# Kernel tuning notes

Measured on AMD Instinct MI355X. Metric: run time of the kernel, lower is better.

The kernel has to match this reference:

```python
import jax, jax.numpy as jnp
import numpy as np

EPS = 1e-5

def _bn(x, gamma, beta, axes):
    # batch-norm with batch statistics (torch training-mode forward, biased var)
    mu = jnp.mean(x, axis=axes, keepdims=True)
    var = jnp.var(x, axis=axes, keepdims=True)
    shape = [1] * x.ndim
    shape[1] = -1  # channel dim is axis 1
    return (x - mu) * jax.lax.rsqrt(var + EPS) * gamma.reshape(shape) + beta.reshape(shape)

def setup_inputs() -> dict:
    key = jax.random.key(0)
    k1, k2, k3, k4, k5 = jax.random.split(key, 5)
    N, H, D, L, M, C = 8, 8, 64, 1024, 1024, 64
    scale = 1.0 / np.sqrt(D)
    return {
        "query": jax.random.normal(k1, (N, H, D, L), dtype=jnp.float32) * scale,
        "key": jax.random.normal(k2, (N, H, D, M), dtype=jnp.float32) * scale,
        "value": jax.random.normal(k3, (N, H, C, M), dtype=jnp.float32),
        "gamma_sim": jnp.ones((H,), dtype=jnp.float32),
        "beta_sim": jnp.zeros((H,), dtype=jnp.float32),
        "gamma_v": jnp.ones((H * C,), dtype=jnp.float32),
        "beta_v": jnp.zeros((H * C,), dtype=jnp.float32),
    }

def reference(query, key, value, gamma_sim, beta_sim, gamma_v, beta_v):
    N, H, D, L = query.shape
    C = value.shape[2]
    # QK^T -> [N, H, L, M]
    logits = jnp.einsum('bhdl,bhdm->bhlm', query, key)
    # BatchNorm2d over channel=head: stats over (N, L, M)
    logits = _bn(logits, gamma_sim, beta_sim, axes=(0, 2, 3))
    # softmax in fp32 (autocast(enabled=False) + .float())
    weights = jax.nn.softmax(logits.astype(jnp.float32), axis=-1)
    # AV -> [N, H, D_v, L] then flatten heads
    rv = jnp.einsum('bhlm,bhdm->bhdl', weights, value).reshape(N, H * C, L)
    # BatchNorm1d over channel: stats over (N, L)
    rv = _bn(rv, gamma_v, beta_v, axes=(0, 2))
    # torch F.gelu default is exact (erf-based)
    return jax.nn.gelu(rv, approximate=False)
```

## Files before the change

### kernel.cpp

```cpp
#include <hip/hip_runtime.h>
#include <hip/hip_bf16.h>
#include <math.h>


typedef __attribute__((ext_vector_type(4)))  float    f32x4;
typedef __attribute__((ext_vector_type(16))) float    f32x16;
typedef __attribute__((ext_vector_type(8)))  __bf16   bf16x8;
typedef __attribute__((ext_vector_type(8)))  short    s16x8;
typedef __attribute__((ext_vector_type(4)))  short    s16x4;
typedef __attribute__((ext_vector_type(2)))  unsigned u32x2;
typedef __attribute__((ext_vector_type(4)))  unsigned u32x4;

#define KT_OFF 0u
#define VB_OFF (8u*1024u*1024u)
#define P1_OFF (16u*1024u*1024u)
#define RS_OFF (24u*1024u*1024u)
#define SPLIT_WS_NEED (24u*1024u*1024u + 512u*1024u + 4096u)

static __device__ __forceinline__ short bf16s(float f) {
  return __builtin_bit_cast(short, (__bf16)f);
}
static __device__ __forceinline__ unsigned pkbf(float lo, float hi) {
  unsigned l = (unsigned)__builtin_bit_cast(unsigned short, (__bf16)lo);
  unsigned h = (unsigned)__builtin_bit_cast(unsigned short, (__bf16)hi);
  return l | (h << 16);
}
static __device__ __forceinline__ float bf2f(short s) {
  return __builtin_bit_cast(float, ((unsigned)(unsigned short)s) << 16);
}
static __device__ __forceinline__ bf16x8 cvt8(const float* p) {
  f32x4 a = *(const f32x4*)p;
  f32x4 b = *(const f32x4*)(p + 4);
  bf16x8 r;
  r[0]=(__bf16)a[0]; r[1]=(__bf16)a[1]; r[2]=(__bf16)a[2]; r[3]=(__bf16)a[3];
  r[4]=(__bf16)b[0]; r[5]=(__bf16)b[1]; r[6]=(__bf16)b[2]; r[7]=(__bf16)b[3];
  return r;
}
static __device__ __forceinline__ f32x16 z16() {
  f32x16 z;
  #pragma unroll
  for (int i = 0; i < 16; ++i) z[i] = 0.f;
  return z;
}
static __device__ __forceinline__ bf16x8 mk8(unsigned a, unsigned b, unsigned c, unsigned d) {
  u32x4 u; u[0]=a; u[1]=b; u[2]=c; u[3]=d;
  return __builtin_bit_cast(bf16x8, u);
}
static __device__ __forceinline__ void gll16(const void* g, void* l) {
  __builtin_amdgcn_global_load_lds(
      (const __attribute__((address_space(1))) void*)g,
      (__attribute__((address_space(3))) void*)l, 16, 0, 0);
}

__global__ __launch_bounds__(256) void k0_prep(const float* __restrict__ K,
                                               const float* __restrict__ V,
                                               short* __restrict__ Kt,
                                               short* __restrict__ Vb) {
  int tid = threadIdx.x;
  if (blockIdx.x < 1024) {
    int bh = blockIdx.x >> 4;
    int m0 = (blockIdx.x & 15) << 6;
    __shared__ short tile[64][72];
    int d = tid >> 2;
    #pragma unroll
    for (int it = 0; it < 4; ++it) {
      int mc4 = (tid & 3) + (it << 2);
      const f32x4 v = *(const f32x4*)(K + (((size_t)(bh*64 + d)) << 10) + m0 + (mc4 << 2));
      #pragma unroll
      for (int j = 0; j < 4; ++j) tile[mc4*4 + j][d] = bf16s(v[j]);
    }
    __syncthreads();
    int m = tid >> 2, q = tid & 3;
    s16x8 o0, o1;
    #pragma unroll
    for (int j = 0; j < 8; ++j) { o0[j] = tile[m][q*16 + j]; o1[j] = tile[m][q*16 + 8 + j]; }
    short* dst = Kt + ((size_t)bh << 16) + ((size_t)(m0 + m) << 6) + (q << 4);
    *(s16x8*)dst = o0;
    *(s16x8*)(dst + 8) = o1;
  } else {
    size_t base = ((size_t)(blockIdx.x - 1024)) << 13;
    #pragma unroll
    for (int it = 0; it < 8; ++it) {
      size_t idx = base + ((size_t)it << 10) + (tid << 2);
      f32x4 x = *(const f32x4*)(V + idx);
      s16x4 y;
      #pragma unroll
      for (int j = 0; j < 4; ++j) y[j] = bf16s(x[j]);
      *(s16x4*)(Vb + idx) = y;
    }
  }
}

__global__ __launch_bounds__(512) void k1_gram(const float* __restrict__ Q,
                                               const float* __restrict__ K,
                                               float* __restrict__ ss) {
  int bh = blockIdx.x;
  int tid = threadIdx.x, w = tid >> 6, lane = tid & 63;
  int l31 = lane & 31, hi = lane >> 5;
  const float* qlo = Q + ((size_t)bh << 16) + ((size_t)l31 << 10);
  const float* qhi = qlo + (32u << 10);
  const float* klo = K + ((size_t)bh << 16) + ((size_t)l31 << 10);
  const float* khi = klo + (32u << 10);
  f32x16 gq00 = z16(), gq01 = z16(), gq11 = z16();
  f32x16 gk00 = z16(), gk01 = z16(), gk11 = z16();
  for (int lc = 0; lc < 8; ++lc) {
    int loff = (w << 7) + (lc << 4) + (hi << 3);
    bf16x8 aql = cvt8(qlo + loff), aqh = cvt8(qhi + loff);
    bf16x8 akl = cvt8(klo + loff), akh = cvt8(khi + loff);
    gq00 = __builtin_amdgcn_mfma_f32_32x32x16_bf16(aql, aql, gq00, 0, 0, 0);
    gq01 = __builtin_amdgcn_mfma_f32_32x32x16_bf16(aql, aqh, gq01, 0, 0, 0);
    gq11 = __builtin_amdgcn_mfma_f32_32x32x16_bf16(aqh, aqh, gq11, 0, 0, 0);
    gk00 = __builtin_amdgcn_mfma_f32_32x32x16_bf16(akl, akl, gk00, 0, 0, 0);
    gk01 = __builtin_amdgcn_mfma_f32_32x32x16_bf16(akl, akh, gk01, 0, 0, 0);
    gk11 = __builtin_amdgcn_mfma_f32_32x32x16_bf16(akh, akh, gk11, 0, 0, 0);
  }
  __shared__ float RQ[8][64][16];
  __shared__ float RK[8][64][16];
  float part = 0.f;
  #define K1_REDUCE(GQ_, GK_, WT_)                                          \
    __syncthreads();                                                        \
    _Pragma("unroll")                                                       \
    for (int r = 0; r < 16; ++r) { RQ[w][lane][r] = GQ_[r]; RK[w][lane][r] = GK_[r]; } \
    __syncthreads();                                                        \
    if (tid < 256) {                                                        \
      int e = tid & 63, rq = (tid >> 6) << 2;                               \
      _Pragma("unroll")                                                     \
      for (int j = 0; j < 4; ++j) {                                         \
        int r = rq + j;                                                     \
        float aq = 0.f, ak = 0.f;                                           \
        _Pragma("unroll")                                                   \
        for (int ww = 0; ww < 8; ++ww) { aq += RQ[ww][e][r]; ak += RK[ww][e][r]; } \
        part += (WT_) * aq * ak;                                            \
      }                                                                     \
    }
  K1_REDUCE(gq00, gk00, 1.0f)
  K1_REDUCE(gq01, gk01, 2.0f)
  K1_REDUCE(gq11, gk11, 1.0f)
  #undef K1_REDUCE
  #pragma unroll
  for (int off = 32; off > 0; off >>= 1) part += __shfl_down(part, off, 64);
  __shared__ float red[8];
  __syncthreads();
  if (lane == 0) red[w] = part;
  __syncthreads();
  if (tid == 0) {
    float s = 0.f;
    #pragma unroll
    for (int ww = 0; ww < 8; ++ww) s += red[ww];
    ss[bh] = s;
  }
}

template<bool SPLIT>
__global__ __launch_bounds__(256) void k2_attn(const float* __restrict__ Q,
                                               const short* __restrict__ Kt,
                                               const short* __restrict__ Vbf,
                                               const float* __restrict__ ss,
                                               const float* __restrict__ gsim,
                                               float* __restrict__ rv,
                                               short* __restrict__ p1,
                                               float* __restrict__ rsp) {
  __shared__ short ldsK[2][4096];
  __shared__ short ldsV[2][4096];
  int b = blockIdx.x;
  int bh   = (b & 7) + (((b >> 3) & 7) << 3);
  int rest = b >> 6;
  int slab  = SPLIT ? (rest >> 1) : rest;
  int mh    = SPLIT ? (rest & 1) : 0;
  int tbase = mh << 3;
  const int TT = SPLIT ? 8 : 16;
  int l0 = slab << 7;
  int tid = threadIdx.x, w = tid >> 6, lane = tid & 63;
  int l31 = lane & 31, hi = lane >> 5;
  int lq = l0 + (w << 5) + l31;

  int h = bh & 7;
  float ssum = 0.f;
  #pragma unroll
  for (int nb = 0; nb < 8; ++nb) ssum += ss[(nb << 3) + h];
  float scf = gsim[h] * rsqrtf(ssum * (1.0f / 8388608.0f) + 1e-5f) * 1.44269504089f;

  const short* ktb = Kt  + ((size_t)bh << 16);
  const short* vbb = Vbf + ((size_t)bh << 16);
  const float* qb  = Q   + ((size_t)bh << 16) + lq;

  bf16x8 qf[4];
  #pragma unroll
  for (int kc = 0; kc < 4; ++kc) {
    bf16x8 f;
    #pragma unroll
    for (int i = 0; i < 8; ++i)
      f[i] = (__bf16)(qb[(size_t)((kc << 4) + (hi << 3) + i) << 10] * scf);
    qf[kc] = f;
  }

  int koff[2][4], voff[2][2][2];
  #pragma unroll
  for (int mt = 0; mt < 2; ++mt) {
    int mrow = (mt << 5) + l31;
    #pragma unroll
    for (int kc = 0; kc < 4; ++kc) {
      int chunk = (kc << 1) + hi;
      koff[mt][kc] = mrow*128 + ((chunk << 4) ^ ((mrow & 7) << 4));
    }
    #pragma unroll
    for (int cz = 0; cz < 2; ++cz) {
      int crow = (cz << 5) + l31;
      #pragma unroll
      for (int j = 0; j < 2; ++j) {
        int chunk = (mt << 2) + (j << 1) + hi;
        voff[mt][cz][j] = crow*128 + ((chunk << 4) ^ ((crow & 7) << 4));
      }
    }
  }

  {
    int m0 = tbase << 6;
    #pragma unroll
    for (int p = 0; p < 2; ++p) {
      int idx = (p << 8) + tid, row = idx >> 3, ch = idx & 7;
      gll16(ktb + ((size_t)(m0 + row) << 6) + ((ch ^ (row & 7)) << 3), &ldsK[0][idx << 3]);
      gll16(vbb + ((size_t)row << 10) + m0 + ((ch ^ (row & 7)) << 3), &ldsV[0][idx << 3]);
    }
  }
  __syncthreads();

  f32x16 o0 = z16(), o1 = z16();
  float rsum = 0.f;

  for (int t = 0; t < TT; ++t) {
    int cur = t & 1, nxt = cur ^ 1;
    if (t < TT - 1) {
      int m1 = (tbase + t + 1) << 6;
      #pragma unroll
      for (int p = 0; p < 2; ++p) {
        int idx = (p << 8) + tid, row = idx >> 3, ch = idx & 7;
        gll16(ktb + ((size_t)(m1 + row) << 6) + ((ch ^ (row & 7)) << 3), &ldsK[nxt][idx << 3]);
        gll16(vbb + ((size_t)row << 10) + m1 + ((ch ^ (row & 7)) << 3), &ldsV[nxt][idx << 3]);
      }
    }
    #pragma unroll
    for (int mt = 0; mt < 2; ++mt) {
      f32x16 s = z16();
      __builtin_amdgcn_s_setprio(1);
      #pragma unroll
      for (int kc = 0; kc < 4; ++kc) {
        bf16x8 af = *(bf16x8*)((char*)&ldsK[cur][0] + koff[mt][kc]);
        s = __builtin_amdgcn_mfma_f32_32x32x16_bf16(af, qf[kc], s, 0, 0, 0);
      }
      __builtin_amdgcn_s_setprio(0);
      float p[16];
      #pragma unroll
      for (int r = 0; r < 16; ++r) { p[r] = __builtin_amdgcn_exp2f(s[r]); rsum += p[r]; }
      unsigned dw[8];
      #pragma unroll
      for (int j = 0; j < 8; ++j) dw[j] = pkbf(p[2*j], p[2*j+1]);
      u32x2 a0 = __builtin_amdgcn_permlane32_swap(dw[0], dw[2], false, false);
      u32x2 a1 = __builtin_amdgcn_permlane32_swap(dw[1], dw[3], false, false);
      u32x2 a2 = __builtin_amdgcn_permlane32_swap(dw[4], dw[6], false, false);
      u32x2 a3 = __builtin_amdgcn_permlane32_swap(dw[5], dw[7], false, false);
      bf16x8 pb0 = mk8(a0[0], a1[0], a0[1], a1[1]);
      bf16x8 pb1 = mk8(a2[0], a3[0], a2[1], a3[1]);
      __builtin_amdgcn_s_setprio(1);
      {
        bf16x8 va0 = *(bf16x8*)((char*)&ldsV[cur][0] + voff[mt][0][0]);
        o0 = __builtin_amdgcn_mfma_f32_32x32x16_bf16(va0, pb0, o0, 0, 0, 0);
        bf16x8 va1 = *(bf16x8*)((char*)&ldsV[cur][0] + voff[mt][0][1]);
        o0 = __builtin_amdgcn_mfma_f32_32x32x16_bf16(va1, pb1, o0, 0, 0, 0);
      }
      {
        bf16x8 va0 = *(bf16x8*)((char*)&ldsV[cur][0] + voff[mt][1][0]);
        o1 = __builtin_amdgcn_mfma_f32_32x32x16_bf16(va0, pb0, o1, 0, 0, 0);
        bf16x8 va1 = *(bf16x8*)((char*)&ldsV[cur][0] + voff[mt][1][1]);
        o1 = __builtin_amdgcn_mfma_f32_32x32x16_bf16(va1, pb1, o1, 0, 0, 0);
      }
      __builtin_amdgcn_s_setprio(0);
    }
    __syncthreads();
  }

  float tot = rsum + __shfl_xor(rsum, 32, 64);
  if constexpr (!SPLIT) {
    float inv = 1.0f / tot;
    #pragma unroll
    for (int r = 0; r < 16; ++r) {
      int cr = (r & 3) + ((r >> 2) << 3) + (hi << 2);
      rv[((size_t)(bh*64 + cr) << 10) + lq] = o0[r] * inv;
    }
    #pragma unroll
    for (int r = 0; r < 16; ++r) {
      int cr = 32 + (r & 3) + ((r >> 2) << 3) + (hi << 2);
      rv[((size_t)(bh*64 + cr) << 10) + lq] = o1[r] * inv;
    }
  } else {
    if (mh == 0) {
      #pragma unroll
      for (int r = 0; r < 16; ++r) {
        int cr = (r & 3) + ((r >> 2) << 3) + (hi << 2);
        rv[((size_t)(bh*64 + cr) << 10) + lq] = o0[r];
      }
      #pragma unroll
      for (int r = 0; r < 16; ++r) {
        int cr = 32 + (r & 3) + ((r >> 2) << 3) + (hi << 2);
        rv[((size_t)(bh*64 + cr) << 10) + lq] = o1[r];
      }
    } else {
      #pragma unroll
      for (int r = 0; r < 16; ++r) {
        int cr = (r & 3) + ((r >> 2) << 3) + (hi << 2);
        p1[((size_t)(bh*64 + cr) << 10) + lq] = bf16s(o0[r]);
      }
      #pragma unroll
      for (int r = 0; r < 16; ++r) {
        int cr = 32 + (r & 3) + ((r >> 2) << 3) + (hi << 2);
        p1[((size_t)(bh*64 + cr) << 10) + lq] = bf16s(o1[r]);
      }
    }
    if (hi == 0) rsp[(mh << 16) + (bh << 10) + lq] = tot;
  }
}

template<bool SPLIT>
__global__ __launch_bounds__(256) void k34_bn_gelu(const float* rv,
                                                   const short* __restrict__ p1,
                                                   const float* __restrict__ rsp,
                                                   const float* __restrict__ gamma_v,
                                                   const float* __restrict__ beta_v,
                                                   float* out) {
  int ch = blockIdx.x;
  int h  = ch >> 6;
  int tid = threadIdx.x, w = tid >> 6, lane = tid & 63;
  f32x4 xr[8];
  float s = 0.f, s2 = 0.f;
  #pragma unroll
  for (int b = 0; b < 8; ++b) {
    size_t roff = (((size_t)(b*512 + ch)) << 10) + (tid << 2);
    f32x4 x = *(const f32x4*)(rv + roff);
    if constexpr (SPLIT) {
      s16x4 pp = *(const s16x4*)(p1 + roff);
      size_t soff = (((size_t)(b*8 + h)) << 10) + (tid << 2);
      f32x4 r0 = *(const f32x4*)(rsp + soff);
      f32x4 r1 = *(const f32x4*)(rsp + 65536 + soff);
      #pragma unroll
      for (int j = 0; j < 4; ++j)
        x[j] = (x[j] + bf2f(pp[j])) / (r0[j] + r1[j]);
    }
    xr[b] = x;
    #pragma unroll
    for (int j = 0; j < 4; ++j) { s += x[j]; s2 += x[j]*x[j]; }
  }
  #pragma unroll
  for (int off = 32; off > 0; off >>= 1) { s += __shfl_down(s, off, 64); s2 += __shfl_down(s2, off, 64); }
  __shared__ float red0[4], red1[4];
  __shared__ float ab[2];
  if (lane == 0) { red0[w] = s; red1[w] = s2; }
  __syncthreads();
  if (tid == 0) {
    float S  = red0[0] + red0[1] + red0[2] + red0[3];
    float S2 = red1[0] + red1[1] + red1[2] + red1[3];
    float mean = S * (1.0f / 8192.0f);
    float var  = S2 * (1.0f / 8192.0f) - mean * mean;
    float a = gamma_v[ch] * rsqrtf(var + 1e-5f);
    ab[0] = a; ab[1] = beta_v[ch] - mean * a;
  }
  __syncthreads();
  float a = ab[0], bb = ab[1];
  #pragma unroll
  for (int b = 0; b < 8; ++b) {
    size_t off = (((size_t)(b*512 + ch)) << 10) + (tid << 2);
    f32x4 y;
    #pragma unroll
    for (int j = 0; j < 4; ++j) {
      float v = a * xr[b][j] + bb;
      y[j] = 0.5f * v * (1.0f + erff(v * 0.70710678118f));
    }
    *(f32x4*)(out + off) = y;
  }
}

extern "C" void kernel_launch(void* const* d_in, const int* in_sizes, int n_in,
                              void* d_out, int out_size, void* d_ws, size_t ws_size,
                              hipStream_t stream) {
  const float* q        = (const float*)d_in[0];
  const float* k        = (const float*)d_in[1];
  const float* v        = (const float*)d_in[2];
  const float* gamma_s  = (const float*)d_in[3];
  const float* gamma_v  = (const float*)d_in[5];
  const float* beta_v   = (const float*)d_in[6];
  float* out = (float*)d_out;
  char*  ws  = (char*)d_ws;
  short* kt  = (short*)(ws + KT_OFF);
  short* vbf = (short*)(ws + VB_OFF);
  short* p1  = (short*)(ws + P1_OFF);
  float* rsp = (float*)(ws + RS_OFF);

  const bool split_ok = ws_size >= (size_t)SPLIT_WS_NEED;
  size_t tail = split_ok ? (size_t)(24u*1024u*1024u + 512u*1024u)
                         : (size_t)(16u*1024u*1024u);
  float* ss = (float*)(ws + tail);

  k0_prep<<<1536, 256, 0, stream>>>(k, v, kt, vbf);
  k1_gram<<<64, 512, 0, stream>>>(q, k, ss);
  if (split_ok) {
    k2_attn<true ><<<1024, 256, 0, stream>>>(q, kt, vbf, ss, gamma_s, out, p1, rsp);
    k34_bn_gelu<true ><<<512, 256, 0, stream>>>(out, p1, rsp, gamma_v, beta_v, out);
  } else {
    k2_attn<false><<<512, 256, 0, stream>>>(q, kt, vbf, ss, gamma_s, out, p1, rsp);
    k34_bn_gelu<false><<<512, 256, 0, stream>>>(out, p1, rsp, gamma_v, beta_v, out);
  }
}
```

Measured before the change: 76.24 us.

## Split Gram-matrix stats kernel across L-slices with a second reduction kernel

Replaces the 64-block Gram kernel, which computes Q·Qᵀ and K·Kᵀ for the BN variance statistics, with a 512-block kernel. Each block handles one eighth of the L dimension and writes partial Gram matrices to workspace. A small follow-up kernel sums the partials and forms the Frobenius dot products per head. The aim is to fill more CUs in a step that used to be latency-bound, at the cost of an extra launch and extra workspace traffic.

```diff
diff --git a/kernel.cpp b/kernel.cpp
--- a/kernel.cpp
+++ b/kernel.cpp
@@ -15,7 +15,9 @@
 #define VB_OFF (8u*1024u*1024u)
 #define P1_OFF (16u*1024u*1024u)
 #define RS_OFF (24u*1024u*1024u)
+#define GM_OFF (32u*1024u*1024u)
 #define SPLIT_WS_NEED (24u*1024u*1024u + 512u*1024u + 4096u)
+#define GRAM2_WS_NEED (48u*1024u*1024u)
 
 static __device__ __forceinline__ short bf16s(float f) {
   return __builtin_bit_cast(short, (__bf16)f);
@@ -89,6 +91,81 @@
       *(s16x4*)(Vb + idx) = y;
     }
   }
+}
+
+__global__ __launch_bounds__(256) void k1a_gram(const float* __restrict__ Q,
+                                                const float* __restrict__ K,
+                                                float* __restrict__ gm) {
+  int bh = blockIdx.x >> 3, sl = blockIdx.x & 7;
+  int tid = threadIdx.x, w = tid >> 6, lane = tid & 63;
+  int l31 = lane & 31, hi = lane >> 5;
+  const float* qlo = Q + ((size_t)bh << 16) + ((size_t)l31 << 10);
+  const float* qhi = qlo + (32u << 10);
+  const float* klo = K + ((size_t)bh << 16) + ((size_t)l31 << 10);
+  const float* khi = klo + (32u << 10);
+  f32x16 gq00 = z16(), gq01 = z16(), gq11 = z16();
+  f32x16 gk00 = z16(), gk01 = z16(), gk11 = z16();
+  #pragma unroll
+  for (int lc = 0; lc < 2; ++lc) {
+    int loff = (sl << 7) + (w << 5) + (lc << 4) + (hi << 3);
+    bf16x8 aql = cvt8(qlo + loff), aqh = cvt8(qhi + loff);
+    bf16x8 akl = cvt8(klo + loff), akh = cvt8(khi + loff);
+    gq00 = __builtin_amdgcn_mfma_f32_32x32x16_bf16(aql, aql, gq00, 0, 0, 0);
+    gq01 = __builtin_amdgcn_mfma_f32_32x32x16_bf16(aql, aqh, gq01, 0, 0, 0);
+    gq11 = __builtin_amdgcn_mfma_f32_32x32x16_bf16(aqh, aqh, gq11, 0, 0, 0);
+    gk00 = __builtin_amdgcn_mfma_f32_32x32x16_bf16(akl, akl, gk00, 0, 0, 0);
+    gk01 = __builtin_amdgcn_mfma_f32_32x32x16_bf16(akl, akh, gk01, 0, 0, 0);
+    gk11 = __builtin_amdgcn_mfma_f32_32x32x16_bf16(akh, akh, gk11, 0, 0, 0);
+  }
+  __shared__ float RQ[4][64][16];
+  __shared__ float RK[4][64][16];
+  float* gout = gm + ((size_t)blockIdx.x * 6144u);
+  #define K1A_RED(GQ_, GK_, TI_)                                            \
+    __syncthreads();                                                        \
+    _Pragma("unroll")                                                       \
+    for (int r = 0; r < 16; ++r) { RQ[w][lane][r] = GQ_[r]; RK[w][lane][r] = GK_[r]; } \
+    __syncthreads();                                                        \
+    {                                                                       \
+      int e = tid & 63, rq = (tid >> 6) << 2;                               \
+      f32x4 aq, ak;                                                         \
+      _Pragma("unroll")                                                     \
+      for (int j = 0; j < 4; ++j) {                                         \
+        int r = rq + j;                                                     \
+        aq[j] = RQ[0][e][r] + RQ[1][e][r] + RQ[2][e][r] + RQ[3][e][r];      \
+        ak[j] = RK[0][e][r] + RK[1][e][r] + RK[2][e][r] + RK[3][e][r];      \
+      }                                                                     \
+      *(f32x4*)(gout + (TI_)*1024 + (e << 4) + rq) = aq;                    \
+      *(f32x4*)(gout + ((TI_) + 3)*1024 + (e << 4) + rq) = ak;              \
+    }
+  K1A_RED(gq00, gk00, 0)
+  K1A_RED(gq01, gk01, 1)
+  K1A_RED(gq11, gk11, 2)
+  #undef K1A_RED
+}
+
+__global__ __launch_bounds__(256) void k1b_dot(const float* __restrict__ gm,
+                                               float* __restrict__ ss) {
+  int bh = blockIdx.x;
+  int tid = threadIdx.x, w = tid >> 6, lane = tid & 63;
+  float part = 0.f;
+  #pragma unroll
+  for (int t = 0; t < 3; ++t) {
+    f32x4 aq = {0.f, 0.f, 0.f, 0.f}, ak = {0.f, 0.f, 0.f, 0.f};
+    #pragma unroll
+    for (int s = 0; s < 8; ++s) {
+      const float* base = gm + ((size_t)((bh << 3) + s) * 6144u) + (size_t)t*1024u + (tid << 2);
+      aq += *(const f32x4*)base;
+      ak += *(const f32x4*)(base + 3*1024);
+    }
+    float d = aq[0]*ak[0] + aq[1]*ak[1] + aq[2]*ak[2] + aq[3]*ak[3];
+    part += (t == 1) ? 2.0f * d : d;
+  }
+  #pragma unroll
+  for (int off = 32; off > 0; off >>= 1) part += __shfl_down(part, off, 64);
+  __shared__ float red[4];
+  if (lane == 0) red[w] = part;
+  __syncthreads();
+  if (tid == 0) ss[bh] = red[0] + red[1] + red[2] + red[3];
 }
 
 __global__ __launch_bounds__(512) void k1_gram(const float* __restrict__ Q,
@@ -393,14 +470,21 @@
   short* vbf = (short*)(ws + VB_OFF);
   short* p1  = (short*)(ws + P1_OFF);
   float* rsp = (float*)(ws + RS_OFF);
+  float* gm  = (float*)(ws + GM_OFF);
 
   const bool split_ok = ws_size >= (size_t)SPLIT_WS_NEED;
+  const bool gram2_ok = ws_size >= (size_t)GRAM2_WS_NEED;
   size_t tail = split_ok ? (size_t)(24u*1024u*1024u + 512u*1024u)
                          : (size_t)(16u*1024u*1024u);
   float* ss = (float*)(ws + tail);
 
   k0_prep<<<1536, 256, 0, stream>>>(k, v, kt, vbf);
-  k1_gram<<<64, 512, 0, stream>>>(q, k, ss);
+  if (gram2_ok) {
+    k1a_gram<<<512, 256, 0, stream>>>(q, k, gm);
+    k1b_dot <<<64, 256, 0, stream>>>(gm, ss);
+  } else {
+    k1_gram<<<64, 512, 0, stream>>>(q, k, ss);
+  }
   if (split_ok) {
     k2_attn<true ><<<1024, 256, 0, stream>>>(q, kt, vbf, ss, gamma_s, out, p1, rsp);
     k34_bn_gelu<true ><<<512, 256, 0, stream>>>(out, p1, rsp, gamma_v, beta_v, out);
```

After: 73.17 us (median of 2 runs). 1.04x faster.
